# Optimization experiments

Measured on AMD Instinct MI355X. Metric: run time of the kernel, lower is better.

Reference implementation:

```python
import jax, jax.numpy as jnp
import numpy as np

NUM_HEADS = 16
NUM_GROUPS = 2
HEAD_DIM = 128  # in_features // num_heads = 2048 // 16
MAX_POS = 512 + 256 + 256  # MAX_SEQ_LEN + SHARED_SLOTS + OUTPUT_SLOTS


def _rope_tables():
    inv_freq = 1.0 / 10000 ** (jnp.arange(0, HEAD_DIM, 2) / HEAD_DIM)
    t = jnp.arange(MAX_POS)
    freqs = jnp.outer(t, inv_freq)
    freqs = jnp.concatenate([freqs, freqs], axis=-1)  # [MAX_POS, HEAD_DIM]
    return jnp.sin(freqs), jnp.cos(freqs)


def _rotate_half(x):
    h = x.shape[-1] // 2
    x1, x2 = x[..., :h], x[..., h:]
    return jnp.concatenate([-x2, x1], axis=-1)


def setup_inputs() -> dict:
    key = jax.random.key(0)
    ks = jax.random.split(key, 5)
    b, s, d = 4, 1024, 2048
    kvd = NUM_GROUPS * HEAD_DIM
    sc = 1.0 / np.sqrt(d).astype(np.float32)
    return {
        "x": jax.random.normal(ks[0], (b, s, d), jnp.float32),
        "Wq": jax.random.normal(ks[1], (d, d), jnp.float32) * sc,
        "bq": jnp.zeros((d,), jnp.float32),
        "Wk": jax.random.normal(ks[2], (d, kvd), jnp.float32) * sc,
        "bk": jnp.zeros((kvd,), jnp.float32),
        "Wv": jax.random.normal(ks[3], (d, kvd), jnp.float32) * sc,
        "bv": jnp.zeros((kvd,), jnp.float32),
        "Wo": jax.random.normal(ks[4], (d, d), jnp.float32) * sc,
        "bo": jnp.zeros((d,), jnp.float32),
    }


def reference(x, Wq, bq, Wk, bk, Wv, bv, Wo, bo):
    b, s, d = x.shape
    sin, cos = _rope_tables()
    # original: sin_cached[q_pos, None, :] broadcasts over (b, s, heads, head_dim)
    sin = sin[:s][None, :, None, :]
    cos = cos[:s][None, :, None, :]

    q = (x @ Wq + bq).reshape(b, s, NUM_HEADS, HEAD_DIM)
    k = (x @ Wk + bk).reshape(b, s, NUM_GROUPS, HEAD_DIM)
    v = (x @ Wv + bv).reshape(b, s, NUM_GROUPS, HEAD_DIM)

    q = q * cos + _rotate_half(q) * sin
    k = k * cos + _rotate_half(k) * sin

    # GQA: avoid materializing expanded K/V by grouping the head dim of q.
    r = NUM_HEADS // NUM_GROUPS  # repeats per group
    qg = q.reshape(b, s, NUM_GROUPS, r, HEAD_DIM)
    scale = HEAD_DIM ** -0.5
    scores = jnp.einsum('bsgrd,btgd->bgrst', qg, k) * scale
    attn = jax.nn.softmax(scores, axis=-1)
    out = jnp.einsum('bgrst,btgd->bsgrd', attn, v).reshape(b, s, d)
    return out @ Wo + bo
```

## Files before the change

### kernel.cpp

```cpp
#include <hip/hip_runtime.h>
#include <hip/hip_bf16.h>
#include <hip/hip_fp16.h>
#include <math.h>

#define BATCH   4
#define SEQ     1024
#define DMODEL  2048
#define NHEADS  16
#define NGROUPS 2
#define HDIM    128
#define ROWS    (BATCH * SEQ)
#define NQKV    2560

typedef float    f32x4 __attribute__((ext_vector_type(4)));
typedef _Float16 f16x8 __attribute__((ext_vector_type(8)));

__device__ __forceinline__ void glds16(const void* g, void* s) {
    __builtin_amdgcn_global_load_lds(
        (__attribute__((address_space(1))) void*)g,
        (__attribute__((address_space(3))) void*)s, 16, 0, 0);
}

__device__ __forceinline__ float red16_max(float v) {
    v = fmaxf(v, __int_as_float(__builtin_amdgcn_mov_dpp(__float_as_int(v), 0xB1, 0xF, 0xF, true)));
    v = fmaxf(v, __int_as_float(__builtin_amdgcn_mov_dpp(__float_as_int(v), 0x4E, 0xF, 0xF, true)));
    v = fmaxf(v, __int_as_float(__builtin_amdgcn_mov_dpp(__float_as_int(v), 0x124, 0xF, 0xF, true)));
    v = fmaxf(v, __int_as_float(__builtin_amdgcn_mov_dpp(__float_as_int(v), 0x128, 0xF, 0xF, true)));
    return v;
}
__device__ __forceinline__ float red16_sum(float v) {
    v += __int_as_float(__builtin_amdgcn_mov_dpp(__float_as_int(v), 0xB1, 0xF, 0xF, true));
    v += __int_as_float(__builtin_amdgcn_mov_dpp(__float_as_int(v), 0x4E, 0xF, 0xF, true));
    v += __int_as_float(__builtin_amdgcn_mov_dpp(__float_as_int(v), 0x124, 0xF, 0xF, true));
    v += __int_as_float(__builtin_amdgcn_mov_dpp(__float_as_int(v), 0x128, 0xF, 0xF, true));
    return v;
}

__global__ void rope_table_kernel(float* __restrict__ sin_t, float* __restrict__ cos_t) {
    int idx = blockIdx.x * 256 + threadIdx.x;
    int p = idx >> 6, j = idx & 63;
    float inv = powf(10000.0f, -(float)j * (1.0f / 64.0f));
    float f = (float)p * inv;
    sin_t[idx] = sinf(f);
    cos_t[idx] = cosf(f);
}

__global__ void convert_x_kernel(const float* __restrict__ x, _Float16* __restrict__ xo) {
    int i = (blockIdx.x * 256 + threadIdx.x) * 8;
    float v[8];
    *reinterpret_cast<float4*>(&v[0]) = *reinterpret_cast<const float4*>(x + i);
    *reinterpret_cast<float4*>(&v[4]) = *reinterpret_cast<const float4*>(x + i + 4);
    f16x8 h;
#pragma unroll
    for (int j = 0; j < 8; ++j) h[j] = (_Float16)v[j];
    *reinterpret_cast<f16x8*>(xo + i) = h;
}

__global__ __launch_bounds__(256)
void transpose_w_kernel(const float* __restrict__ W, int ldw,
                        _Float16* __restrict__ dst, int drow0, int K) {
    __shared__ float tile[64][65];
    int n0 = blockIdx.x * 64, k0 = blockIdx.y * 64;
#pragma unroll
    for (int it = 0; it < 16; ++it) {
        int e = it * 256 + threadIdx.x;
        int r = e >> 6, c = e & 63;
        tile[r][c] = W[(size_t)(k0 + r) * ldw + n0 + c];
    }
    __syncthreads();
#pragma unroll
    for (int it = 0; it < 16; ++it) {
        int e = it * 256 + threadIdx.x;
        int nr = e >> 6, kc = e & 63;
        dst[(size_t)(drow0 + n0 + nr) * K + k0 + kc] = (_Float16)tile[kc][nr];
    }
}

__global__ void bias_cat_kernel(const float* __restrict__ bq, const float* __restrict__ bk,
                                const float* __restrict__ bv, float* __restrict__ bc) {
    int i = blockIdx.x * 256 + threadIdx.x;
    if (i >= NQKV) return;
    bc[i] = (i < 2048) ? bq[i] : ((i < 2304) ? bk[i - 2048] : bv[i - 2304]);
}

template<int OUT_HALF>
__global__ __launch_bounds__(256, 3)
void gemm_fp16_kernel(const _Float16* __restrict__ A, const _Float16* __restrict__ Bt,
                      const float* __restrict__ bias, void* __restrict__ Cout,
                      int M, int N, int K) {
    __shared__ __align__(16) _Float16 lds[16384];
    _Float16* As = lds;
    _Float16* Bs = lds + 8192;

    const int tid  = threadIdx.x;
    const int lane = tid & 63;
    const int w    = tid >> 6;
    const int nbn  = N >> 7;
    const int nwg  = gridDim.x;
    const int cpx  = nwg >> 3;
    const int bid  = blockIdx.x;
    const int swz  = (bid & 7) * cpx + (bid >> 3);
    const int row0 = (swz / nbn) << 7;
    const int col0 = (swz % nbn) << 7;
    const int wr   = (w >> 1) << 6;
    const int wc   = (w & 1) << 6;

    const f32x4 fz = {0.f, 0.f, 0.f, 0.f};
    f32x4 acc[4][4];
#pragma unroll
    for (int i = 0; i < 4; ++i)
#pragma unroll
        for (int j = 0; j < 4; ++j) acc[i][j] = fz;

    for (int k0 = 0; k0 < K; k0 += 64) {
        __syncthreads();
#pragma unroll
        for (int it = 0; it < 4; ++it) {
            int chunk = it * 256 + tid;
            int trow  = chunk >> 3;
            int jp    = chunk & 7;
            int j     = jp ^ (trow & 7);
            size_t aoff = (size_t)(row0 + trow) * K + k0 + j * 8;
            size_t boff = (size_t)(col0 + trow) * K + k0 + j * 8;
            int ldst = (it * 256 + (tid & 192)) * 16;
            glds16(A  + aoff, (char*)As + ldst);
            glds16(Bt + boff, (char*)Bs + ldst);
        }
        __syncthreads();

#pragma unroll
        for (int ks = 0; ks < 2; ++ks) {
            f16x8 a4[4], b4[4];
            int ja = ks * 4 + (lane >> 4);
#pragma unroll
            for (int i = 0; i < 4; ++i) {
                int ar = wr + i * 16 + (lane & 15);
                a4[i] = *reinterpret_cast<const f16x8*>(
                    (const char*)As + ar * 128 + ((ja ^ (ar & 7)) << 4));
                int br = wc + i * 16 + (lane & 15);
                b4[i] = *reinterpret_cast<const f16x8*>(
                    (const char*)Bs + br * 128 + ((ja ^ (br & 7)) << 4));
            }
#pragma unroll
            for (int i = 0; i < 4; ++i)
#pragma unroll
                for (int j = 0; j < 4; ++j)
                    acc[i][j] = __builtin_amdgcn_mfma_f32_16x16x32_f16(a4[i], b4[j], acc[i][j], 0, 0, 0);
        }
    }

    float bv4[4];
#pragma unroll
    for (int j = 0; j < 4; ++j) bv4[j] = bias[col0 + wc + j * 16 + (lane & 15)];
#pragma unroll
    for (int i = 0; i < 4; ++i)
#pragma unroll
        for (int j = 0; j < 4; ++j)
#pragma unroll
            for (int r = 0; r < 4; ++r) {
                int grow = row0 + wr + i * 16 + ((lane >> 4) << 2) + r;
                int gcol = col0 + wc + j * 16 + (lane & 15);
                float v = acc[i][j][r] + bv4[j];
                if (OUT_HALF)
                    ((_Float16*)Cout)[(size_t)grow * N + gcol] = (_Float16)v;
                else
                    ((float*)Cout)[(size_t)grow * N + gcol] = v;
            }
}

__global__ void rope_k_kernel(const _Float16* __restrict__ qkv,
                              const float* __restrict__ sin_t, const float* __restrict__ cos_t,
                              _Float16* __restrict__ kh) {
    int idx = blockIdx.x * 256 + threadIdx.x;
    int jc = idx & 7, t = idx >> 3;
    int j0 = jc * 8;
    int row = t >> 1, g = t & 1;
    int b = row >> 10, s = row & 1023;
    const _Float16* src = qkv + (size_t)row * NQKV + 2048 + g * HDIM;
    _Float16* dst = kh + ((size_t)(b * NGROUPS + g) * SEQ + s) * HDIM;
    f16x8 x1 = *reinterpret_cast<const f16x8*>(src + j0);
    f16x8 x2 = *reinterpret_cast<const f16x8*>(src + j0 + 64);
    float cc[8], ss[8];
    *reinterpret_cast<float4*>(&cc[0]) = *reinterpret_cast<const float4*>(cos_t + s * 64 + j0);
    *reinterpret_cast<float4*>(&cc[4]) = *reinterpret_cast<const float4*>(cos_t + s * 64 + j0 + 4);
    *reinterpret_cast<float4*>(&ss[0]) = *reinterpret_cast<const float4*>(sin_t + s * 64 + j0);
    *reinterpret_cast<float4*>(&ss[4]) = *reinterpret_cast<const float4*>(sin_t + s * 64 + j0 + 4);
    f16x8 o1, o2;
#pragma unroll
    for (int j = 0; j < 8; ++j) {
        float f1 = (float)x1[j], f2 = (float)x2[j];
        o1[j] = (_Float16)(f1 * cc[j] - f2 * ss[j]);
        o2[j] = (_Float16)(f2 * cc[j] + f1 * ss[j]);
    }
    *reinterpret_cast<f16x8*>(dst + j0)      = o1;
    *reinterpret_cast<f16x8*>(dst + j0 + 64) = o2;
}

__global__ __launch_bounds__(256)
void transpose_v_kernel(const _Float16* __restrict__ qkv, _Float16* __restrict__ vt) {
    __shared__ _Float16 tile[64][72];
    int s0 = blockIdx.x * 64, d0 = blockIdx.y * 64, bg = blockIdx.z;
    int b = bg >> 1, g = bg & 1;
#pragma unroll
    for (int it = 0; it < 2; ++it) {
        int c = it * 256 + threadIdx.x;
        int r = c >> 3, cc = (c & 7) * 8;
        f16x8 v = *reinterpret_cast<const f16x8*>(
            qkv + (size_t)(b * SEQ + s0 + r) * NQKV + 2304 + g * HDIM + d0 + cc);
#pragma unroll
        for (int j = 0; j < 8; ++j) tile[r][cc + j] = v[j];
    }
    __syncthreads();
#pragma unroll
    for (int it = 0; it < 2; ++it) {
        int c = it * 256 + threadIdx.x;
        int dr = c >> 3, sc = (c & 7) * 8;
        f16x8 o;
#pragma unroll
        for (int j = 0; j < 8; ++j) o[j] = tile[sc + j][dr];
        *reinterpret_cast<f16x8*>(vt + ((size_t)bg * HDIM + d0 + dr) * SEQ + s0 + sc) = o;
    }
}

__global__ __launch_bounds__(256, 2)
void attn_kernel(const _Float16* __restrict__ qkv, const _Float16* __restrict__ kh,
                 const _Float16* __restrict__ vt,
                 const float* __restrict__ sin_t, const float* __restrict__ cos_t,
                 _Float16* __restrict__ ao) {
    __shared__ __align__(16) char smem[81920];

    const int tid = threadIdx.x, lane = tid & 63, w = tid >> 6;
    const int qt0 = blockIdx.x << 7;
    const int h = blockIdx.y, b = blockIdx.z;
    const int g = h >> 3;
    const _Float16* kbase = kh + (size_t)(b * NGROUPS + g) * SEQ * HDIM;
    const _Float16* vbase = vt + (size_t)(b * NGROUPS + g) * HDIM * SEQ;

    {
        char* Kb = smem;
        char* Vb = smem + 16384;
#pragma unroll
        for (int it = 0; it < 4; ++it) {
            int c = it * 256 + tid;
            int row = c >> 4, jc = c & 15;
            int sj = jc ^ (row & 7);
            glds16((const char*)(kbase + (size_t)row * HDIM) + (sj << 4),
                   Kb + (it * 256 + (tid & 192)) * 16);
        }
#pragma unroll
        for (int it = 0; it < 4; ++it) {
            int c = it * 256 + tid;
            int d = c >> 3, jc = c & 7;
            int sj = jc ^ (d & 7);
            glds16((const char*)(vbase + (size_t)d * SEQ) + (sj << 4),
                   Vb + (it * 256 + (tid & 192)) * 16);
        }
    }

    const int sl = lane >> 4;
    f16x8 af[2][4];
#pragma unroll
    for (int m = 0; m < 2; ++m) {
        int srow = qt0 + w * 32 + m * 16 + (lane & 15);
        const _Float16* qrp = qkv + (size_t)(b * SEQ + srow) * NQKV + h * HDIM;
#pragma unroll
        for (int ks = 0; ks < 4; ++ks)
            af[m][ks] = *reinterpret_cast<const f16x8*>(qrp + (ks * 4 + sl) * 8);
        const float qsc = 0.08838834764831845f;
#pragma unroll
        for (int ks = 0; ks < 2; ++ks) {
            int d0 = (ks * 4 + sl) * 8;
            float cc[8], ss[8];
            *reinterpret_cast<float4*>(&cc[0]) = *reinterpret_cast<const float4*>(cos_t + srow * 64 + d0);
            *reinterpret_cast<float4*>(&cc[4]) = *reinterpret_cast<const float4*>(cos_t + srow * 64 + d0 + 4);
            *reinterpret_cast<float4*>(&ss[0]) = *reinterpret_cast<const float4*>(sin_t + srow * 64 + d0);
            *reinterpret_cast<float4*>(&ss[4]) = *reinterpret_cast<const float4*>(sin_t + srow * 64 + d0 + 4);
#pragma unroll
            for (int j = 0; j < 8; ++j) {
                float f1 = (float)af[m][ks][j], f2 = (float)af[m][ks + 2][j];
                af[m][ks][j]     = (_Float16)((f1 * cc[j] - f2 * ss[j]) * qsc);
                af[m][ks + 2][j] = (_Float16)((f2 * cc[j] + f1 * ss[j]) * qsc);
            }
        }
    }

    float m_run[2][4], l_run[2][4];
#pragma unroll
    for (int m = 0; m < 2; ++m)
#pragma unroll
        for (int r = 0; r < 4; ++r) { m_run[m][r] = -1e30f; l_run[m][r] = 0.f; }
    const f32x4 fz = {0.f, 0.f, 0.f, 0.f};
    f32x4 oacc[2][8];
#pragma unroll
    for (int m = 0; m < 2; ++m)
#pragma unroll
        for (int i = 0; i < 8; ++i) oacc[m][i] = fz;

    char* Pw = smem + 65536 + w * 4096;
    const int prow = lane & 15;

    int cur = 0;
    for (int t = 0; t < SEQ / 64; ++t) {
        char* Kb = smem + (cur << 15);
        char* Vb = Kb + 16384;
        if (t < SEQ / 64 - 1) {
            char* Kn = smem + ((cur ^ 1) << 15);
            char* Vn = Kn + 16384;
            int t0n = (t + 1) << 6;
#pragma unroll
            for (int it = 0; it < 4; ++it) {
                int c = it * 256 + tid;
                int row = c >> 4, jc = c & 15;
                int sj = jc ^ (row & 7);
                glds16((const char*)(kbase + (size_t)(t0n + row) * HDIM) + (sj << 4),
                       Kn + (it * 256 + (tid & 192)) * 16);
            }
#pragma unroll
            for (int it = 0; it < 4; ++it) {
                int c = it * 256 + tid;
                int d = c >> 3, jc = c & 7;
                int sj = jc ^ (d & 7);
                glds16((const char*)(vbase + (size_t)d * SEQ + t0n) + (sj << 4),
                       Vn + (it * 256 + (tid & 192)) * 16);
            }
            asm volatile("s_waitcnt vmcnt(8)" ::: "memory");
        } else {
            asm volatile("s_waitcnt vmcnt(0)" ::: "memory");
        }
        asm volatile("s_barrier" ::: "memory");

        f32x4 sacc[2][4];
#pragma unroll
        for (int m = 0; m < 2; ++m)
#pragma unroll
            for (int i = 0; i < 4; ++i) sacc[m][i] = fz;
#pragma unroll
        for (int ks = 0; ks < 4; ++ks) {
#pragma unroll
            for (int nf = 0; nf < 4; ++nf) {
                int trow = nf * 16 + (lane & 15);
                f16x8 bf = *reinterpret_cast<const f16x8*>(
                    Kb + trow * 256 + (((ks * 4 + (lane >> 4)) ^ (trow & 7)) << 4));
                sacc[0][nf] = __builtin_amdgcn_mfma_f32_16x16x32_f16(af[0][ks], bf, sacc[0][nf], 0, 0, 0);
                sacc[1][nf] = __builtin_amdgcn_mfma_f32_16x16x32_f16(af[1][ks], bf, sacc[1][nf], 0, 0, 0);
            }
        }

        float pm[2][4];
        float growth = -1e30f;
#pragma unroll
        for (int m = 0; m < 2; ++m)
#pragma unroll
            for (int r = 0; r < 4; ++r) {
                float v = fmaxf(fmaxf(sacc[m][0][r], sacc[m][1][r]),
                                fmaxf(sacc[m][2][r], sacc[m][3][r]));
                v = red16_max(v);
                pm[m][r] = v;
                growth = fmaxf(growth, v - m_run[m][r]);
            }
        if (__any(growth > 8.0f)) {
            float scl[2][4];
#pragma unroll
            for (int m = 0; m < 2; ++m)
#pragma unroll
                for (int r = 0; r < 4; ++r) {
                    float mn = fmaxf(m_run[m][r], pm[m][r]);
                    scl[m][r] = __expf(m_run[m][r] - mn);
                    m_run[m][r] = mn;
                    l_run[m][r] *= scl[m][r];
                }
#pragma unroll
            for (int m = 0; m < 2; ++m)
#pragma unroll
                for (int i = 0; i < 8; ++i) {
                    f32x4 o = oacc[m][i];
                    o[0] *= scl[m][0]; o[1] *= scl[m][1];
                    o[2] *= scl[m][2]; o[3] *= scl[m][3];
                    oacc[m][i] = o;
                }
        }
#pragma unroll
        for (int m = 0; m < 2; ++m)
#pragma unroll
            for (int r = 0; r < 4; ++r) {
                float ps = 0.f;
#pragma unroll
                for (int nf = 0; nf < 4; ++nf) {
                    float p = __expf(sacc[m][nf][r] - m_run[m][r]);
                    sacc[m][nf][r] = p;
                    ps += p;
                }
                l_run[m][r] += red16_sum(ps);
            }

#pragma unroll
        for (int m = 0; m < 2; ++m)
#pragma unroll
            for (int nf = 0; nf < 4; ++nf)
#pragma unroll
                for (int r = 0; r < 4; ++r) {
                    int pr = m * 16 + ((lane >> 4) << 2) + r;
                    int pc = nf * 16 + (lane & 15);
                    int byte = pr * 128 + ((pc * 2) ^ ((pr & 7) << 4));
                    *reinterpret_cast<_Float16*>(Pw + byte) = (_Float16)sacc[m][nf][r];
                }

#pragma unroll
        for (int ks = 0; ks < 2; ++ks) {
            int chP = ks * 4 + (lane >> 4);
            f16x8 pa[2];
#pragma unroll
            for (int m = 0; m < 2; ++m)
                pa[m] = *reinterpret_cast<const f16x8*>(
                    Pw + (m * 16 + prow) * 128 + ((chP ^ (prow & 7)) << 4));
#pragma unroll
            for (int nf = 0; nf < 8; ++nf) {
                int vrow = nf * 16 + (lane & 15);
                f16x8 vf = *reinterpret_cast<const f16x8*>(
                    Vb + vrow * 128 + (((ks * 4 + (lane >> 4)) ^ (vrow & 7)) << 4));
                oacc[0][nf] = __builtin_amdgcn_mfma_f32_16x16x32_f16(pa[0], vf, oacc[0][nf], 0, 0, 0);
                oacc[1][nf] = __builtin_amdgcn_mfma_f32_16x16x32_f16(pa[1], vf, oacc[1][nf], 0, 0, 0);
            }
        }

        asm volatile("s_barrier" ::: "memory");
        cur ^= 1;
    }

#pragma unroll
    for (int m = 0; m < 2; ++m)
#pragma unroll
        for (int nf = 0; nf < 8; ++nf)
#pragma unroll
            for (int r = 0; r < 4; ++r) {
                int qr  = qt0 + w * 32 + m * 16 + ((lane >> 4) << 2) + r;
                int col = h * HDIM + nf * 16 + (lane & 15);
                float v = oacc[m][nf][r] / l_run[m][r];
                ao[(size_t)(b * SEQ + qr) * DMODEL + col] = (_Float16)v;
            }
}

extern "C" void kernel_launch(void* const* d_in, const int* in_sizes, int n_in,
                              void* d_out, int out_size, void* d_ws, size_t ws_size,
                              hipStream_t stream) {
    const float* x  = (const float*)d_in[0];
    const float* Wq = (const float*)d_in[1];
    const float* bq = (const float*)d_in[2];
    const float* Wk = (const float*)d_in[3];
    const float* bk = (const float*)d_in[4];
    const float* Wv = (const float*)d_in[5];
    const float* bv = (const float*)d_in[6];
    const float* Wo = (const float*)d_in[7];
    const float* bo = (const float*)d_in[8];
    float* out = (float*)d_out;

    char* ws = (char*)d_ws;
    _Float16* xs     = (_Float16*)(ws);
    _Float16* wqkv16 = (_Float16*)(ws + 16777216);
    _Float16* wot16  = (_Float16*)(ws + 27262976);
    _Float16* qkv16  = (_Float16*)(ws + 35651584);
    _Float16* khb    = (_Float16*)(ws + 56623104);
    _Float16* vtb    = (_Float16*)(ws + 58720256);
    float*    sint   = (float*)(ws + 60817408);
    float*    cost   = (float*)(ws + 61079552);
    float*    bias_c = (float*)(ws + 61341696);
    _Float16* ao = xs;

    rope_table_kernel<<<SEQ * 64 / 256, 256, 0, stream>>>(sint, cost);
    convert_x_kernel<<<ROWS * DMODEL / 8 / 256, 256, 0, stream>>>(x, xs);
    transpose_w_kernel<<<dim3(32, 32), 256, 0, stream>>>(Wq, DMODEL, wqkv16, 0, DMODEL);
    transpose_w_kernel<<<dim3(4, 32),  256, 0, stream>>>(Wk, 256,    wqkv16, 2048, DMODEL);
    transpose_w_kernel<<<dim3(4, 32),  256, 0, stream>>>(Wv, 256,    wqkv16, 2304, DMODEL);
    transpose_w_kernel<<<dim3(32, 32), 256, 0, stream>>>(Wo, DMODEL, wot16,  0, DMODEL);
    bias_cat_kernel<<<10, 256, 0, stream>>>(bq, bk, bv, bias_c);

    gemm_fp16_kernel<1><<<(ROWS / 128) * (NQKV / 128), 256, 0, stream>>>(
        xs, wqkv16, bias_c, qkv16, ROWS, NQKV, DMODEL);

    rope_k_kernel<<<(ROWS * NGROUPS * 8) / 256, 256, 0, stream>>>(qkv16, sint, cost, khb);
    transpose_v_kernel<<<dim3(SEQ / 64, HDIM / 64, BATCH * NGROUPS), 256, 0, stream>>>(qkv16, vtb);

    attn_kernel<<<dim3(SEQ / 128, NHEADS, BATCH), 256, 0, stream>>>(
        qkv16, khb, vtb, sint, cost, ao);

    gemm_fp16_kernel<0><<<(ROWS / 128) * (DMODEL / 128), 256, 0, stream>>>(
        ao, wot16, bo, out, ROWS, DMODEL, DMODEL);
}
```

Before: 293.4 us.

## Fuse prep kernels and single-buffer attention with exp2 softmax for higher occupancy

Merges the rope-table and bias-concat kernels, merges the four weight transposes into one launch, and fuses K RoPE with the V transpose, cutting the number of kernel launches. The attention kernel drops double-buffered K/V staging for a single buffer plus __syncthreads, shrinking LDS so launch bounds can go to 3 blocks per CU. It also folds log2(e) into the Q scale and uses exp2, raises the rescale threshold to match the base-2 scores, and defers the cross-lane row-sum reduction to the epilogue. The trade-off is that K/V loads no longer overlap compute within a block, so latency hiding now depends on the extra occupancy.

```diff
diff --git a/kernel.cpp b/kernel.cpp
--- a/kernel.cpp
+++ b/kernel.cpp
@@ -36,13 +36,22 @@
     return v;
 }
 
-__global__ void rope_table_kernel(float* __restrict__ sin_t, float* __restrict__ cos_t) {
-    int idx = blockIdx.x * 256 + threadIdx.x;
-    int p = idx >> 6, j = idx & 63;
-    float inv = powf(10000.0f, -(float)j * (1.0f / 64.0f));
-    float f = (float)p * inv;
-    sin_t[idx] = sinf(f);
-    cos_t[idx] = cosf(f);
+__global__ void prep_const_kernel(float* __restrict__ sin_t, float* __restrict__ cos_t,
+                                  const float* __restrict__ bq, const float* __restrict__ bk,
+                                  const float* __restrict__ bv, float* __restrict__ bc) {
+    int bid = blockIdx.x;
+    if (bid < 256) {
+        int idx = bid * 256 + threadIdx.x;
+        int p = idx >> 6, j = idx & 63;
+        float inv = powf(10000.0f, -(float)j * (1.0f / 64.0f));
+        float f = (float)p * inv;
+        sin_t[idx] = sinf(f);
+        cos_t[idx] = cosf(f);
+    } else {
+        int i = (bid - 256) * 256 + threadIdx.x;
+        if (i < NQKV)
+            bc[i] = (i < 2048) ? bq[i] : ((i < 2304) ? bk[i - 2048] : bv[i - 2304]);
+    }
 }
 
 __global__ void convert_x_kernel(const float* __restrict__ x, _Float16* __restrict__ xo) {
@@ -57,10 +66,17 @@
 }
 
 __global__ __launch_bounds__(256)
-void transpose_w_kernel(const float* __restrict__ W, int ldw,
-                        _Float16* __restrict__ dst, int drow0, int K) {
+void transpose_w_all_kernel(const float* __restrict__ Wq, const float* __restrict__ Wk,
+                            const float* __restrict__ Wv, const float* __restrict__ Wo,
+                            _Float16* __restrict__ wqkv, _Float16* __restrict__ wot) {
     __shared__ float tile[64][65];
-    int n0 = blockIdx.x * 64, k0 = blockIdx.y * 64;
+    int bx = blockIdx.x;
+    const float* W; int ldw, drow0, nb; _Float16* dst;
+    if (bx < 32)      { W = Wq; ldw = DMODEL; dst = wqkv; drow0 = 0;    nb = bx; }
+    else if (bx < 36) { W = Wk; ldw = 256;    dst = wqkv; drow0 = 2048; nb = bx - 32; }
+    else if (bx < 40) { W = Wv; ldw = 256;    dst = wqkv; drow0 = 2304; nb = bx - 36; }
+    else              { W = Wo; ldw = DMODEL; dst = wot;  drow0 = 0;    nb = bx - 40; }
+    int n0 = nb * 64, k0 = blockIdx.y * 64;
 #pragma unroll
     for (int it = 0; it < 16; ++it) {
         int e = it * 256 + threadIdx.x;
@@ -72,15 +88,8 @@
     for (int it = 0; it < 16; ++it) {
         int e = it * 256 + threadIdx.x;
         int nr = e >> 6, kc = e & 63;
-        dst[(size_t)(drow0 + n0 + nr) * K + k0 + kc] = (_Float16)tile[kc][nr];
-    }
-}
-
-__global__ void bias_cat_kernel(const float* __restrict__ bq, const float* __restrict__ bk,
-                                const float* __restrict__ bv, float* __restrict__ bc) {
-    int i = blockIdx.x * 256 + threadIdx.x;
-    if (i >= NQKV) return;
-    bc[i] = (i < 2048) ? bq[i] : ((i < 2304) ? bk[i - 2048] : bv[i - 2304]);
+        dst[(size_t)(drow0 + n0 + nr) * DMODEL + k0 + kc] = (_Float16)tile[kc][nr];
+    }
 }
 
 template<int OUT_HALF>
@@ -168,66 +177,72 @@
             }
 }
 
-__global__ void rope_k_kernel(const _Float16* __restrict__ qkv,
-                              const float* __restrict__ sin_t, const float* __restrict__ cos_t,
-                              _Float16* __restrict__ kh) {
-    int idx = blockIdx.x * 256 + threadIdx.x;
-    int jc = idx & 7, t = idx >> 3;
-    int j0 = jc * 8;
-    int row = t >> 1, g = t & 1;
-    int b = row >> 10, s = row & 1023;
-    const _Float16* src = qkv + (size_t)row * NQKV + 2048 + g * HDIM;
-    _Float16* dst = kh + ((size_t)(b * NGROUPS + g) * SEQ + s) * HDIM;
-    f16x8 x1 = *reinterpret_cast<const f16x8*>(src + j0);
-    f16x8 x2 = *reinterpret_cast<const f16x8*>(src + j0 + 64);
-    float cc[8], ss[8];
-    *reinterpret_cast<float4*>(&cc[0]) = *reinterpret_cast<const float4*>(cos_t + s * 64 + j0);
-    *reinterpret_cast<float4*>(&cc[4]) = *reinterpret_cast<const float4*>(cos_t + s * 64 + j0 + 4);
-    *reinterpret_cast<float4*>(&ss[0]) = *reinterpret_cast<const float4*>(sin_t + s * 64 + j0);
-    *reinterpret_cast<float4*>(&ss[4]) = *reinterpret_cast<const float4*>(sin_t + s * 64 + j0 + 4);
-    f16x8 o1, o2;
-#pragma unroll
-    for (int j = 0; j < 8; ++j) {
-        float f1 = (float)x1[j], f2 = (float)x2[j];
-        o1[j] = (_Float16)(f1 * cc[j] - f2 * ss[j]);
-        o2[j] = (_Float16)(f2 * cc[j] + f1 * ss[j]);
-    }
-    *reinterpret_cast<f16x8*>(dst + j0)      = o1;
-    *reinterpret_cast<f16x8*>(dst + j0 + 64) = o2;
-}
-
 __global__ __launch_bounds__(256)
-void transpose_v_kernel(const _Float16* __restrict__ qkv, _Float16* __restrict__ vt) {
+void prep_kv_kernel(const _Float16* __restrict__ qkv,
+                    const float* __restrict__ sin_t, const float* __restrict__ cos_t,
+                    _Float16* __restrict__ kh, _Float16* __restrict__ vt) {
     __shared__ _Float16 tile[64][72];
-    int s0 = blockIdx.x * 64, d0 = blockIdx.y * 64, bg = blockIdx.z;
+    int s0 = blockIdx.x * 64, bg = blockIdx.y;
     int b = bg >> 1, g = bg & 1;
+
 #pragma unroll
     for (int it = 0; it < 2; ++it) {
-        int c = it * 256 + threadIdx.x;
-        int r = c >> 3, cc = (c & 7) * 8;
-        f16x8 v = *reinterpret_cast<const f16x8*>(
-            qkv + (size_t)(b * SEQ + s0 + r) * NQKV + 2304 + g * HDIM + d0 + cc);
-#pragma unroll
-        for (int j = 0; j < 8; ++j) tile[r][cc + j] = v[j];
-    }
-    __syncthreads();
-#pragma unroll
-    for (int it = 0; it < 2; ++it) {
-        int c = it * 256 + threadIdx.x;
-        int dr = c >> 3, sc = (c & 7) * 8;
-        f16x8 o;
-#pragma unroll
-        for (int j = 0; j < 8; ++j) o[j] = tile[sc + j][dr];
-        *reinterpret_cast<f16x8*>(vt + ((size_t)bg * HDIM + d0 + dr) * SEQ + s0 + sc) = o;
-    }
-}
-
-__global__ __launch_bounds__(256, 2)
+        int u = it * 256 + threadIdx.x;
+        int r = u >> 3, jc = u & 7;
+        int s = s0 + r;
+        int j0 = jc * 8;
+        const _Float16* src = qkv + (size_t)(b * SEQ + s) * NQKV + 2048 + g * HDIM;
+        _Float16* dst = kh + ((size_t)bg * SEQ + s) * HDIM;
+        f16x8 x1 = *reinterpret_cast<const f16x8*>(src + j0);
+        f16x8 x2 = *reinterpret_cast<const f16x8*>(src + j0 + 64);
+        float cc[8], ss[8];
+        *reinterpret_cast<float4*>(&cc[0]) = *reinterpret_cast<const float4*>(cos_t + s * 64 + j0);
+        *reinterpret_cast<float4*>(&cc[4]) = *reinterpret_cast<const float4*>(cos_t + s * 64 + j0 + 4);
+        *reinterpret_cast<float4*>(&ss[0]) = *reinterpret_cast<const float4*>(sin_t + s * 64 + j0);
+        *reinterpret_cast<float4*>(&ss[4]) = *reinterpret_cast<const float4*>(sin_t + s * 64 + j0 + 4);
+        f16x8 o1, o2;
+#pragma unroll
+        for (int j = 0; j < 8; ++j) {
+            float f1 = (float)x1[j], f2 = (float)x2[j];
+            o1[j] = (_Float16)(f1 * cc[j] - f2 * ss[j]);
+            o2[j] = (_Float16)(f2 * cc[j] + f1 * ss[j]);
+        }
+        *reinterpret_cast<f16x8*>(dst + j0)      = o1;
+        *reinterpret_cast<f16x8*>(dst + j0 + 64) = o2;
+    }
+
+#pragma unroll
+    for (int half = 0; half < 2; ++half) {
+        int d0 = half * 64;
+        __syncthreads();
+#pragma unroll
+        for (int it = 0; it < 2; ++it) {
+            int c = it * 256 + threadIdx.x;
+            int r = c >> 3, cc = (c & 7) * 8;
+            f16x8 v = *reinterpret_cast<const f16x8*>(
+                qkv + (size_t)(b * SEQ + s0 + r) * NQKV + 2304 + g * HDIM + d0 + cc);
+#pragma unroll
+            for (int j = 0; j < 8; ++j) tile[r][cc + j] = v[j];
+        }
+        __syncthreads();
+#pragma unroll
+        for (int it = 0; it < 2; ++it) {
+            int c = it * 256 + threadIdx.x;
+            int dr = c >> 3, sc = (c & 7) * 8;
+            f16x8 o;
+#pragma unroll
+            for (int j = 0; j < 8; ++j) o[j] = tile[sc + j][dr];
+            *reinterpret_cast<f16x8*>(vt + ((size_t)bg * HDIM + d0 + dr) * SEQ + s0 + sc) = o;
+        }
+    }
+}
+
+__global__ __launch_bounds__(256, 3)
 void attn_kernel(const _Float16* __restrict__ qkv, const _Float16* __restrict__ kh,
                  const _Float16* __restrict__ vt,
                  const float* __restrict__ sin_t, const float* __restrict__ cos_t,
                  _Float16* __restrict__ ao) {
-    __shared__ __align__(16) char smem[81920];
+    __shared__ __align__(16) char smem[49152];
 
     const int tid = threadIdx.x, lane = tid & 63, w = tid >> 6;
     const int qt0 = blockIdx.x << 7;
@@ -235,27 +250,9 @@
     const int g = h >> 3;
     const _Float16* kbase = kh + (size_t)(b * NGROUPS + g) * SEQ * HDIM;
     const _Float16* vbase = vt + (size_t)(b * NGROUPS + g) * HDIM * SEQ;
-
-    {
-        char* Kb = smem;
-        char* Vb = smem + 16384;
-#pragma unroll
-        for (int it = 0; it < 4; ++it) {
-            int c = it * 256 + tid;
-            int row = c >> 4, jc = c & 15;
-            int sj = jc ^ (row & 7);
-            glds16((const char*)(kbase + (size_t)row * HDIM) + (sj << 4),
-                   Kb + (it * 256 + (tid & 192)) * 16);
-        }
-#pragma unroll
-        for (int it = 0; it < 4; ++it) {
-            int c = it * 256 + tid;
-            int d = c >> 3, jc = c & 7;
-            int sj = jc ^ (d & 7);
-            glds16((const char*)(vbase + (size_t)d * SEQ) + (sj << 4),
-                   Vb + (it * 256 + (tid & 192)) * 16);
-        }
-    }
+    char* Kb = smem;
+    char* Vb = smem + 16384;
+    char* Pw = smem + 32768 + w * 4096;
 
     const int sl = lane >> 4;
     f16x8 af[2][4];
@@ -266,7 +263,7 @@
 #pragma unroll
         for (int ks = 0; ks < 4; ++ks)
             af[m][ks] = *reinterpret_cast<const f16x8*>(qrp + (ks * 4 + sl) * 8);
-        const float qsc = 0.08838834764831845f;
+        const float qsc = 0.12751741f;
 #pragma unroll
         for (int ks = 0; ks < 2; ++ks) {
             int d0 = (ks * 4 + sl) * 8;
@@ -296,38 +293,27 @@
 #pragma unroll
         for (int i = 0; i < 8; ++i) oacc[m][i] = fz;
 
-    char* Pw = smem + 65536 + w * 4096;
     const int prow = lane & 15;
 
-    int cur = 0;
     for (int t = 0; t < SEQ / 64; ++t) {
-        char* Kb = smem + (cur << 15);
-        char* Vb = Kb + 16384;
-        if (t < SEQ / 64 - 1) {
-            char* Kn = smem + ((cur ^ 1) << 15);
-            char* Vn = Kn + 16384;
-            int t0n = (t + 1) << 6;
-#pragma unroll
-            for (int it = 0; it < 4; ++it) {
-                int c = it * 256 + tid;
-                int row = c >> 4, jc = c & 15;
-                int sj = jc ^ (row & 7);
-                glds16((const char*)(kbase + (size_t)(t0n + row) * HDIM) + (sj << 4),
-                       Kn + (it * 256 + (tid & 192)) * 16);
-            }
-#pragma unroll
-            for (int it = 0; it < 4; ++it) {
-                int c = it * 256 + tid;
-                int d = c >> 3, jc = c & 7;
-                int sj = jc ^ (d & 7);
-                glds16((const char*)(vbase + (size_t)d * SEQ + t0n) + (sj << 4),
-                       Vn + (it * 256 + (tid & 192)) * 16);
-            }
-            asm volatile("s_waitcnt vmcnt(8)" ::: "memory");
-        } else {
-            asm volatile("s_waitcnt vmcnt(0)" ::: "memory");
-        }
-        asm volatile("s_barrier" ::: "memory");
+        int t0 = t << 6;
+#pragma unroll
+        for (int it = 0; it < 4; ++it) {
+            int c = it * 256 + tid;
+            int row = c >> 4, jc = c & 15;
+            int sj = jc ^ (row & 7);
+            glds16((const char*)(kbase + (size_t)(t0 + row) * HDIM) + (sj << 4),
+                   Kb + (it * 256 + (tid & 192)) * 16);
+        }
+#pragma unroll
+        for (int it = 0; it < 4; ++it) {
+            int c = it * 256 + tid;
+            int d = c >> 3, jc = c & 7;
+            int sj = jc ^ (d & 7);
+            glds16((const char*)(vbase + (size_t)d * SEQ + t0) + (sj << 4),
+                   Vb + (it * 256 + (tid & 192)) * 16);
+        }
+        __syncthreads();
 
         f32x4 sacc[2][4];
 #pragma unroll
@@ -358,14 +344,14 @@
                 pm[m][r] = v;
                 growth = fmaxf(growth, v - m_run[m][r]);
             }
-        if (__any(growth > 8.0f)) {
+        if (__any(growth > 11.0f)) {
             float scl[2][4];
 #pragma unroll
             for (int m = 0; m < 2; ++m)
 #pragma unroll
                 for (int r = 0; r < 4; ++r) {
                     float mn = fmaxf(m_run[m][r], pm[m][r]);
-                    scl[m][r] = __expf(m_run[m][r] - mn);
+                    scl[m][r] = __builtin_amdgcn_exp2f(m_run[m][r] - mn);
                     m_run[m][r] = mn;
                     l_run[m][r] *= scl[m][r];
                 }
@@ -386,11 +372,11 @@
                 float ps = 0.f;
 #pragma unroll
                 for (int nf = 0; nf < 4; ++nf) {
-                    float p = __expf(sacc[m][nf][r] - m_run[m][r]);
+                    float p = __builtin_amdgcn_exp2f(sacc[m][nf][r] - m_run[m][r]);
                     sacc[m][nf][r] = p;
                     ps += p;
                 }
-                l_run[m][r] += red16_sum(ps);
+                l_run[m][r] += ps;
             }
 
 #pragma unroll
@@ -423,10 +409,15 @@
             }
         }
 
-        asm volatile("s_barrier" ::: "memory");
-        cur ^= 1;
-    }
-
+        __syncthreads();
+    }
+
+    float linv[2][4];
+#pragma unroll
+    for (int m = 0; m < 2; ++m)
+#pragma unroll
+        for (int r = 0; r < 4; ++r)
+            linv[m][r] = 1.0f / red16_sum(l_run[m][r]);
 #pragma unroll
     for (int m = 0; m < 2; ++m)
 #pragma unroll
@@ -435,7 +426,7 @@
             for (int r = 0; r < 4; ++r) {
                 int qr  = qt0 + w * 32 + m * 16 + ((lane >> 4) << 2) + r;
                 int col = h * HDIM + nf * 16 + (lane & 15);
-                float v = oacc[m][nf][r] / l_run[m][r];
+                float v = oacc[m][nf][r] * linv[m][r];
                 ao[(size_t)(b * SEQ + qr) * DMODEL + col] = (_Float16)v;
             }
 }
@@ -466,19 +457,15 @@
     float*    bias_c = (float*)(ws + 61341696);
     _Float16* ao = xs;
 
-    rope_table_kernel<<<SEQ * 64 / 256, 256, 0, stream>>>(sint, cost);
+    prep_const_kernel<<<266, 256, 0, stream>>>(sint, cost, bq, bk, bv, bias_c);
     convert_x_kernel<<<ROWS * DMODEL / 8 / 256, 256, 0, stream>>>(x, xs);
-    transpose_w_kernel<<<dim3(32, 32), 256, 0, stream>>>(Wq, DMODEL, wqkv16, 0, DMODEL);
-    transpose_w_kernel<<<dim3(4, 32),  256, 0, stream>>>(Wk, 256,    wqkv16, 2048, DMODEL);
-    transpose_w_kernel<<<dim3(4, 32),  256, 0, stream>>>(Wv, 256,    wqkv16, 2304, DMODEL);
-    transpose_w_kernel<<<dim3(32, 32), 256, 0, stream>>>(Wo, DMODEL, wot16,  0, DMODEL);
-    bias_cat_kernel<<<10, 256, 0, stream>>>(bq, bk, bv, bias_c);
+    transpose_w_all_kernel<<<dim3(72, 32), 256, 0, stream>>>(Wq, Wk, Wv, Wo, wqkv16, wot16);
 
     gemm_fp16_kernel<1><<<(ROWS / 128) * (NQKV / 128), 256, 0, stream>>>(
         xs, wqkv16, bias_c, qkv16, ROWS, NQKV, DMODEL);
 
-    rope_k_kernel<<<(ROWS * NGROUPS * 8) / 256, 256, 0, stream>>>(qkv16, sint, cost, khb);
-    transpose_v_kernel<<<dim3(SEQ / 64, HDIM / 64, BATCH * NGROUPS), 256, 0, stream>>>(qkv16, vtb);
+    prep_kv_kernel<<<dim3(SEQ / 64, BATCH * NGROUPS), 256, 0, stream>>>(
+        qkv16, sint, cost, khb, vtb);
 
     attn_kernel<<<dim3(SEQ / 128, NHEADS, BATCH), 256, 0, stream>>>(
         qkv16, khb, vtb, sint, cost, ao);
```

Measured after the change: 341.1 us. 1.16x slower.
